# Kernel tuning notes

Measured on AMD Instinct MI355X. Metric: run time of the kernel, lower is better.

## Reference

```python
import jax, jax.numpy as jnp
import numpy as np

# fp4 e2m1 positive value grid and midpoints between adjacent grid values
_GRID = jnp.array([0.0, 0.5, 1.0, 1.5, 2.0, 3.0, 4.0, 6.0], dtype=jnp.float32)
_MIDS = jnp.array([0.25, 0.75, 1.25, 1.75, 2.5, 3.5, 5.0], dtype=jnp.float32)
BLOCK = 32               # MX block size
E8M0_BIAS = 127
F32_MIN_NORMAL = float(2.0 ** -126)
F4_E2M1_MAX_POW2 = 2     # log2 of largest power-of-two <= 6.0 -> 4.0


def _quantize_fp4(a):
    """Round-to-nearest-even onto the signed e2m1 grid."""
    mag = jnp.clip(jnp.abs(a), 0.0, 6.0)
    idx = jnp.searchsorted(_MIDS, mag, side='left')  # ties round down
    mids_pad = jnp.concatenate([_MIDS, jnp.array([-1.0], jnp.float32)])
    tie = mag == mids_pad[idx]
    idx = jnp.where(tie & (idx % 2 == 1), idx + 1, idx)  # ties-to-even mantissa
    return _GRID[idx] * jnp.where(a < 0, -1.0, 1.0)


def _floor_log2(m):
    """Exact floor(log2(m)) for m > 0, with corrections for fp rounding of log2."""
    e = jnp.floor(jnp.log2(m))
    e = jnp.where(jnp.exp2(e) > m, e - 1.0, e)
    e = jnp.where(jnp.exp2(e + 1.0) <= m, e + 1.0, e)
    return e


def _qdq_mxfp4(x):
    """Quantize-dequantize x to MX fp4_e2m1, block 32, FLOOR scale mode (to_mx + to_dtype)."""
    shp = x.shape
    xb = x.reshape(-1, BLOCK)
    max_abs = jnp.max(jnp.abs(xb), axis=1)
    eps = F32_MIN_NORMAL * (max_abs == 0).astype(jnp.float32)
    pow2 = _floor_log2(max_abs + eps)
    e_unb = jnp.clip(pow2 - F4_E2M1_MAX_POW2, -float(E8M0_BIAS), float(E8M0_BIAS) + 1.0)
    scale = jnp.maximum(jnp.exp2(e_unb), F32_MIN_NORMAL)  # [nblk]
    q = _quantize_fp4(xb / scale[:, None])
    return (q * scale[:, None]).reshape(shp)


def _dequant_weight(weight_packed, weight_scale, out_f, in_f):
    """Unpack uint8-packed fp4 (low nibble first), apply e8m0 block scales."""
    p = weight_packed.astype(jnp.int32)
    low = p & 0xF
    high = (p >> 4) & 0xF
    nib = jnp.stack([low, high], axis=-1).reshape(out_f, in_f)  # interleave low,high
    vals = _GRID[nib & 7] * jnp.where((nib & 8) > 0, -1.0, 1.0)
    s = jnp.exp2(weight_scale.astype(jnp.float32) - E8M0_BIAS)  # get_fp_scale(e8m0)
    return (vals.reshape(-1, BLOCK) * s[:, None]).reshape(out_f, in_f)


def setup_inputs() -> dict:
    key = jax.random.key(0)
    k1, k2, k3 = jax.random.split(key, 3)
    M, IN, OUT = 4096, 4096, 4096
    x = jax.random.normal(k1, (M, IN), dtype=jnp.float32)
    weight_packed = jax.random.randint(k2, (OUT, IN // 2), 0, 256, dtype=jnp.int32)
    weight_scale = jax.random.randint(k3, (OUT * IN // BLOCK,), 0, 135, dtype=jnp.int32)
    return {"x": x, "weight_packed": weight_packed, "weight_scale": weight_scale}


def reference(x, weight_packed, weight_scale):
    out_f = weight_packed.shape[0]
    in_f = weight_packed.shape[1] * 2
    xq = _qdq_mxfp4(x)                                       # qdq_mxfp4(x)
    w_dq = _dequant_weight(weight_packed, weight_scale, out_f, in_f)
    return xq @ w_dq.T                                       # matmul(x, w_dq.t())
```

## Files before the change

kernel.cpp:

```cpp
#include <hip/hip_runtime.h>
#include <stdint.h>

typedef __attribute__((ext_vector_type(4)))  int   intx4;
typedef __attribute__((ext_vector_type(8)))  int   intx8;
typedef __attribute__((ext_vector_type(16))) float floatx16;

#define GLL16(gp, lp)                                                               \
    __builtin_amdgcn_global_load_lds((const __attribute__((address_space(1))) unsigned int*)(gp), \
                                     (__attribute__((address_space(3))) unsigned int*)(lp), 16, 0, 0)
#define GLL4(gp, lp)                                                                \
    __builtin_amdgcn_global_load_lds((const __attribute__((address_space(1))) unsigned int*)(gp), \
                                     (__attribute__((address_space(3))) unsigned int*)(lp), 4, 0, 0)

__device__ __forceinline__ uint32_t enc1(float xv, float inv) {
    float a = fminf(fabsf(xv) * inv, 6.0f);
    int e;
    if (a < 2.0f)      e = (int)rintf(a + a);
    else if (a < 4.0f) e = (int)rintf(a) + 2;
    else               e = (int)rintf(a * 0.5f) + 4;
    return (uint32_t)e | ((__float_as_uint(xv) >> 28) & 8u);
}

__global__ __launch_bounds__(256) void quant_x_kernel(const float* __restrict__ x,
                                                      uint32_t* __restrict__ xq,
                                                      uint8_t* __restrict__ xs) {
    const int gl = blockIdx.x * 256 + threadIdx.x;
    const float4 v = ((const float4*)x)[gl];
    float m = fmaxf(fmaxf(fabsf(v.x), fabsf(v.y)), fmaxf(fabsf(v.z), fabsf(v.w)));
    m = fmaxf(m, __shfl_xor(m, 1));
    m = fmaxf(m, __shfl_xor(m, 2));
    m = fmaxf(m, __shfl_xor(m, 4));
    const unsigned ef = __float_as_uint(m) >> 23;
    const unsigned code = (ef < 3u) ? 1u : (ef - 2u);
    const float inv = __uint_as_float((254u - code) << 23);
    const uint32_t p = enc1(v.x, inv)        | (enc1(v.y, inv) << 4)
                     | (enc1(v.z, inv) << 8) | (enc1(v.w, inv) << 12);
    ((uint16_t*)xq)[gl] = (uint16_t)p;
    if ((gl & 7) == 0) xs[gl >> 3] = (uint8_t)code;
}

__global__ __launch_bounds__(256) void repack_kernel(const int* __restrict__ wp,
                                                     uint32_t* __restrict__ wrep,
                                                     int nwb,
                                                     const uint8_t* __restrict__ xs,
                                                     const int* __restrict__ wsc,
                                                     uint8_t* __restrict__ xs_t,
                                                     uint8_t* __restrict__ ws_t,
                                                     int R, int Ck) {
    const int bid = blockIdx.x;
    const int t = threadIdx.x;
    if (bid < nwb) {
        const int i = bid * 256 + t;
        const int4 p = ((const int4*)wp)[i];
        wrep[i] = (uint32_t)(p.x & 0xFF) | ((uint32_t)(p.y & 0xFF) << 8)
                | ((uint32_t)(p.z & 0xFF) << 16) | ((uint32_t)(p.w & 0xFF) << 24);
        return;
    }
    __shared__ uint8_t raw[128 * 32];
    const int tidx = bid - nwb;
    const int r0 = (tidx & 63) * 128;
    const int c0 = (tidx >> 6) * 32;
    const int r = t >> 1, hf = t & 1;
    if (r0 < R) {
        const uint4 v = *(const uint4*)(xs + (size_t)(r0 + r) * Ck + c0 + hf * 16);
        *(uint4*)(raw + r * 32 + hf * 16) = v;
    } else {
        const size_t base = (size_t)(r0 - R + r) * Ck + c0 + hf * 16;
        uint32_t b[4];
#pragma unroll
        for (int j = 0; j < 4; ++j) {
            const int4 p = *(const int4*)(wsc + base + 4 * j);
            b[j] = (uint32_t)(p.x & 0xFF) | ((uint32_t)(p.y & 0xFF) << 8)
                 | ((uint32_t)(p.z & 0xFF) << 16) | ((uint32_t)(p.w & 0xFF) << 24);
        }
        *(uint4*)(raw + r * 32 + hf * 16) = make_uint4(b[0], b[1], b[2], b[3]);
    }
    __syncthreads();
    const int c = t >> 3, q = t & 7;
    uint32_t d[4];
#pragma unroll
    for (int j = 0; j < 4; ++j) {
        const int mb = q * 16 + j * 4;
        d[j] = (uint32_t)raw[(mb + 0) * 32 + c]
             | ((uint32_t)raw[(mb + 1) * 32 + c] << 8)
             | ((uint32_t)raw[(mb + 2) * 32 + c] << 16)
             | ((uint32_t)raw[(mb + 3) * 32 + c] << 24);
    }
    uint8_t* outp = (r0 < R) ? (xs_t + (size_t)(c0 + c) * R + r0)
                             : (ws_t + (size_t)(c0 + c) * R + (r0 - R));
    *(uint4*)(outp + q * 16) = make_uint4(d[0], d[1], d[2], d[3]);
}

__global__ __launch_bounds__(256) void gemm_mx_kernel(const uint8_t* __restrict__ Apk,
                                                      const uint8_t* __restrict__ Bpk,
                                                      const uint8_t* __restrict__ AsT,
                                                      const uint8_t* __restrict__ BsT,
                                                      float* __restrict__ C,
                                                      int M, int N, int K) {
    __shared__ __align__(16) uint8_t sA[16384];
    __shared__ __align__(16) uint8_t sB[16384];
    __shared__ __align__(16) uint8_t sS[2048];

    const int tid = threadIdx.x;
    const int nwg = gridDim.x * gridDim.y;
    int bid = blockIdx.y * gridDim.x + blockIdx.x;
    bid = (bid & 7) * (nwg >> 3) + (bid >> 3);
    const int bn0 = (bid % gridDim.x) << 7;
    const int bm0 = (bid / gridDim.x) << 7;

    const int wave = tid >> 6;
    const int lane = tid & 63;
    const int wm = (wave >> 1) << 6;
    const int wn = (wave & 1) << 6;
    const int row = lane & 31;
    const int h = lane >> 5;
    const int Kb = K >> 1;

    const uint8_t* Ag[4];
    const uint8_t* Bg[4];
#pragma unroll
    for (int i = 0; i < 4; ++i) {
        const int s = tid + 256 * i;
        const int r = s >> 3;
        const int p = (s & 7) ^ (r & 7);
        Ag[i] = Apk + (size_t)(bm0 + r) * Kb + p * 16;
        Bg[i] = Bpk + (size_t)(bn0 + r) * Kb + p * 16;
    }

    const int st = tid & 127;
    const int sj = st >> 5, si = st & 31;
    const size_t sR = (size_t)((tid < 128) ? M : N);
    const uint8_t* Sg1 = ((tid < 128) ? (AsT + (size_t)sj * M + bm0)
                                      : (BsT + (size_t)sj * N + bn0)) + si * 4;
    const uint8_t* Sg2 = Sg1 + 4 * sR;
    const size_t sAdv = 8 * sR;
    const int soff = ((tid < 128) ? 0 : 1024) + st * 4;

    floatx16 acc[2][2];
#pragma unroll
    for (int a = 0; a < 2; ++a)
#pragma unroll
        for (int b = 0; b < 2; ++b)
#pragma unroll
            for (int r = 0; r < 16; ++r) acc[a][b][r] = 0.f;

    const int nchunk = K >> 8;
    const int ar0 = wm + row, ar1 = wm + 32 + row;
    const int br0 = wn + row, br1 = wn + 32 + row;

    for (int c = 0; c < nchunk; ++c) {
        __syncthreads();
        const size_t koff = (size_t)c << 7;
#pragma unroll
        for (int i = 0; i < 4; ++i) GLL16(Ag[i] + koff, sA + (tid + 256 * i) * 16);
#pragma unroll
        for (int i = 0; i < 4; ++i) GLL16(Bg[i] + koff, sB + (tid + 256 * i) * 16);
        GLL4(Sg1 + (size_t)c * sAdv, sS + soff);
        GLL4(Sg2 + (size_t)c * sAdv, sS + soff + 512);
        __syncthreads();

#pragma unroll
        for (int s = 0; s < 4; ++s) {
            const int kp = 2 * s + h;
            intx4 a4[2], b4[2];
            int sa[2], sb[2];
            a4[0] = *(const intx4*)(sA + ar0 * 128 + ((kp ^ (ar0 & 7)) << 4));
            a4[1] = *(const intx4*)(sA + ar1 * 128 + ((kp ^ (ar1 & 7)) << 4));
            b4[0] = *(const intx4*)(sB + br0 * 128 + ((kp ^ (br0 & 7)) << 4));
            b4[1] = *(const intx4*)(sB + br1 * 128 + ((kp ^ (br1 & 7)) << 4));
            sa[0] = sS[kp * 128 + ar0];
            sa[1] = sS[kp * 128 + ar1];
            sb[0] = sS[1024 + kp * 128 + br0];
            sb[1] = sS[1024 + kp * 128 + br1];
#pragma unroll
            for (int mt = 0; mt < 2; ++mt)
#pragma unroll
                for (int nt = 0; nt < 2; ++nt) {
                    intx8 a8 = {a4[mt][0], a4[mt][1], a4[mt][2], a4[mt][3], 0, 0, 0, 0};
                    intx8 b8 = {b4[nt][0], b4[nt][1], b4[nt][2], b4[nt][3], 0, 0, 0, 0};
                    acc[mt][nt] = __builtin_amdgcn_mfma_scale_f32_32x32x64_f8f6f4(
                        a8, b8, acc[mt][nt], 4, 4, 0, sa[mt], 0, sb[nt]);
                }
        }
    }

#pragma unroll
    for (int mt = 0; mt < 2; ++mt)
#pragma unroll
        for (int nt = 0; nt < 2; ++nt) {
            const int col = bn0 + wn + nt * 32 + row;
#pragma unroll
            for (int g = 0; g < 4; ++g) {
                const int rw = bm0 + wm + mt * 32 + 8 * g + 4 * h;
#pragma unroll
                for (int q = 0; q < 4; ++q)
                    C[(size_t)(rw + q) * N + col] = acc[mt][nt][4 * g + q];
            }
        }
}

extern "C" void kernel_launch(void* const* d_in, const int* in_sizes, int n_in,
                              void* d_out, int out_size, void* d_ws, size_t ws_size,
                              hipStream_t stream) {
    const float* x = (const float*)d_in[0];
    const int* wp = (const int*)d_in[1];
    const int* wsc = (const int*)d_in[2];
    float* out = (float*)d_out;

    const int K = 4096;
    const int M = in_sizes[0] / K;
    const int N = (in_sizes[1] * 2) / K;
    const int kbpr = K / 32;
    const int npack = N * K / 2;

    uint32_t* xq   = (uint32_t*)d_ws;
    uint8_t*  xs   = (uint8_t*)d_ws + (size_t)M * K / 2;
    uint32_t* wrep = (uint32_t*)(xs + (size_t)M * kbpr);
    uint8_t*  xs_t = (uint8_t*)(wrep + (size_t)npack / 4);
    uint8_t*  ws_t = xs_t + (size_t)M * kbpr;

    const int nwb = npack / 4 / 256;
    const int ntb = (2 * M / 128) * (kbpr / 32);

    quant_x_kernel<<<(M * K / 4) / 256, 256, 0, stream>>>(x, xq, xs);
    repack_kernel<<<nwb + ntb, 256, 0, stream>>>(wp, wrep, nwb,
                                                 xs, wsc, xs_t, ws_t, M, kbpr);

    dim3 grid(N / 128, M / 128);
    gemm_mx_kernel<<<grid, 256, 0, stream>>>((const uint8_t*)xq, (const uint8_t*)wrep,
                                             xs_t, ws_t, out, M, N, K);
}
```

Baseline: 199.6 us.

## Interleave scale layout so GEMM loads scales directly into registers

The x scales are now written in an interleaved per-row layout straight from the quantize kernel, so the x-scale transpose pass in the repack kernel goes away. The weight-scale repack produces the same layout. The GEMM reads each lane's scales with one 32-bit global load per 32-row tile per chunk, replacing the LDS staging buffer and byte LDS reads. The grouped block-index swizzle is also removed, which may change L2 reuse across workgroups.

Result: faster. 191.4 us (-4.1%).

```diff
diff --git a/kernel.cpp b/kernel.cpp
--- a/kernel.cpp
+++ b/kernel.cpp
@@ -8,9 +8,6 @@
 #define GLL16(gp, lp)                                                               \
     __builtin_amdgcn_global_load_lds((const __attribute__((address_space(1))) unsigned int*)(gp), \
                                      (__attribute__((address_space(3))) unsigned int*)(lp), 16, 0, 0)
-#define GLL4(gp, lp)                                                                \
-    __builtin_amdgcn_global_load_lds((const __attribute__((address_space(1))) unsigned int*)(gp), \
-                                     (__attribute__((address_space(3))) unsigned int*)(lp), 4, 0, 0)
 
 __device__ __forceinline__ uint32_t enc1(float xv, float inv) {
     float a = fminf(fabsf(xv) * inv, 6.0f);
@@ -23,7 +20,8 @@
 
 __global__ __launch_bounds__(256) void quant_x_kernel(const float* __restrict__ x,
                                                       uint32_t* __restrict__ xq,
-                                                      uint8_t* __restrict__ xs) {
+                                                      uint8_t* __restrict__ xsi,
+                                                      int M) {
     const int gl = blockIdx.x * 256 + threadIdx.x;
     const float4 v = ((const float4*)x)[gl];
     float m = fmaxf(fmaxf(fabsf(v.x), fabsf(v.y)), fmaxf(fabsf(v.z), fabsf(v.w)));
@@ -36,16 +34,19 @@
     const uint32_t p = enc1(v.x, inv)        | (enc1(v.y, inv) << 4)
                      | (enc1(v.z, inv) << 8) | (enc1(v.w, inv) << 12);
     ((uint16_t*)xq)[gl] = (uint16_t)p;
-    if ((gl & 7) == 0) xs[gl >> 3] = (uint8_t)code;
+    if ((gl & 7) == 0) {
+        const int blk = gl >> 3;
+        const int mm = blk >> 7, kb = blk & 127;
+        xsi[(size_t)(kb >> 3) * ((size_t)M * 8) + (size_t)mm * 8
+            + ((kb & 1) << 2) + ((kb & 7) >> 1)] = (uint8_t)code;
+    }
 }
 
 __global__ __launch_bounds__(256) void repack_kernel(const int* __restrict__ wp,
                                                      uint32_t* __restrict__ wrep,
                                                      int nwb,
-                                                     const uint8_t* __restrict__ xs,
                                                      const int* __restrict__ wsc,
-                                                     uint8_t* __restrict__ xs_t,
-                                                     uint8_t* __restrict__ ws_t,
+                                                     uint8_t* __restrict__ ws_i,
                                                      int R, int Ck) {
     const int bid = blockIdx.x;
     const int t = threadIdx.x;
@@ -58,14 +59,11 @@
     }
     __shared__ uint8_t raw[128 * 32];
     const int tidx = bid - nwb;
-    const int r0 = (tidx & 63) * 128;
-    const int c0 = (tidx >> 6) * 32;
-    const int r = t >> 1, hf = t & 1;
-    if (r0 < R) {
-        const uint4 v = *(const uint4*)(xs + (size_t)(r0 + r) * Ck + c0 + hf * 16);
-        *(uint4*)(raw + r * 32 + hf * 16) = v;
-    } else {
-        const size_t base = (size_t)(r0 - R + r) * Ck + c0 + hf * 16;
+    const int n0 = (tidx & 31) * 128;
+    const int c0 = (tidx >> 5) * 32;
+    {
+        const int r = t >> 1, hf = t & 1;
+        const size_t base = (size_t)(n0 + r) * Ck + c0 + hf * 16;
         uint32_t b[4];
 #pragma unroll
         for (int j = 0; j < 4; ++j) {
@@ -76,38 +74,32 @@
         *(uint4*)(raw + r * 32 + hf * 16) = make_uint4(b[0], b[1], b[2], b[3]);
     }
     __syncthreads();
-    const int c = t >> 3, q = t & 7;
-    uint32_t d[4];
-#pragma unroll
-    for (int j = 0; j < 4; ++j) {
-        const int mb = q * 16 + j * 4;
-        d[j] = (uint32_t)raw[(mb + 0) * 32 + c]
-             | ((uint32_t)raw[(mb + 1) * 32 + c] << 8)
-             | ((uint32_t)raw[(mb + 2) * 32 + c] << 16)
-             | ((uint32_t)raw[(mb + 3) * 32 + c] << 24);
-    }
-    uint8_t* outp = (r0 < R) ? (xs_t + (size_t)(c0 + c) * R + r0)
-                             : (ws_t + (size_t)(c0 + c) * R + (r0 - R));
-    *(uint4*)(outp + q * 16) = make_uint4(d[0], d[1], d[2], d[3]);
+    const int ml = t & 127;
+#pragma unroll
+    for (int pp = 0; pp < 2; ++pp) {
+        const int ckl = (t >> 7) + 2 * pp;
+        const int base = ml * 32 + ckl * 8;
+        const uint32_t lo = (uint32_t)raw[base + 0] | ((uint32_t)raw[base + 2] << 8)
+                          | ((uint32_t)raw[base + 4] << 16) | ((uint32_t)raw[base + 6] << 24);
+        const uint32_t hi = (uint32_t)raw[base + 1] | ((uint32_t)raw[base + 3] << 8)
+                          | ((uint32_t)raw[base + 5] << 16) | ((uint32_t)raw[base + 7] << 24);
+        *(uint2*)(ws_i + (size_t)(c0 / 8 + ckl) * ((size_t)R * 8)
+                       + (size_t)(n0 + ml) * 8) = make_uint2(lo, hi);
+    }
 }
 
 __global__ __launch_bounds__(256) void gemm_mx_kernel(const uint8_t* __restrict__ Apk,
                                                       const uint8_t* __restrict__ Bpk,
-                                                      const uint8_t* __restrict__ AsT,
-                                                      const uint8_t* __restrict__ BsT,
+                                                      const uint8_t* __restrict__ Asi,
+                                                      const uint8_t* __restrict__ Bsi,
                                                       float* __restrict__ C,
                                                       int M, int N, int K) {
     __shared__ __align__(16) uint8_t sA[16384];
     __shared__ __align__(16) uint8_t sB[16384];
-    __shared__ __align__(16) uint8_t sS[2048];
 
     const int tid = threadIdx.x;
-    const int nwg = gridDim.x * gridDim.y;
-    int bid = blockIdx.y * gridDim.x + blockIdx.x;
-    bid = (bid & 7) * (nwg >> 3) + (bid >> 3);
-    const int bn0 = (bid % gridDim.x) << 7;
-    const int bm0 = (bid / gridDim.x) << 7;
-
+    const int bm0 = blockIdx.y << 7;
+    const int bn0 = blockIdx.x << 7;
     const int wave = tid >> 6;
     const int lane = tid & 63;
     const int wm = (wave >> 1) << 6;
@@ -127,26 +119,25 @@
         Bg[i] = Bpk + (size_t)(bn0 + r) * Kb + p * 16;
     }
 
-    const int st = tid & 127;
-    const int sj = st >> 5, si = st & 31;
-    const size_t sR = (size_t)((tid < 128) ? M : N);
-    const uint8_t* Sg1 = ((tid < 128) ? (AsT + (size_t)sj * M + bm0)
-                                      : (BsT + (size_t)sj * N + bn0)) + si * 4;
-    const uint8_t* Sg2 = Sg1 + 4 * sR;
-    const size_t sAdv = 8 * sR;
-    const int soff = ((tid < 128) ? 0 : 1024) + st * 4;
-
-    floatx16 acc[2][2];
-#pragma unroll
-    for (int a = 0; a < 2; ++a)
-#pragma unroll
-        for (int b = 0; b < 2; ++b)
-#pragma unroll
-            for (int r = 0; r < 16; ++r) acc[a][b][r] = 0.f;
-
-    const int nchunk = K >> 8;
     const int ar0 = wm + row, ar1 = wm + 32 + row;
     const int br0 = wn + row, br1 = wn + 32 + row;
+
+    const uint8_t* SgA0 = Asi + (size_t)(bm0 + ar0) * 8 + h * 4;
+    const uint8_t* SgA1 = Asi + (size_t)(bm0 + ar1) * 8 + h * 4;
+    const uint8_t* SgB0 = Bsi + (size_t)(bn0 + br0) * 8 + h * 4;
+    const uint8_t* SgB1 = Bsi + (size_t)(bn0 + br1) * 8 + h * 4;
+    const size_t sStepA = (size_t)M * 8;
+    const size_t sStepB = (size_t)N * 8;
+
+    floatx16 acc[2][2];
+#pragma unroll
+    for (int a = 0; a < 2; ++a)
+#pragma unroll
+        for (int b = 0; b < 2; ++b)
+#pragma unroll
+            for (int r = 0; r < 16; ++r) acc[a][b][r] = 0.f;
+
+    const int nchunk = K >> 8;
 
     for (int c = 0; c < nchunk; ++c) {
         __syncthreads();
@@ -155,23 +146,25 @@
         for (int i = 0; i < 4; ++i) GLL16(Ag[i] + koff, sA + (tid + 256 * i) * 16);
 #pragma unroll
         for (int i = 0; i < 4; ++i) GLL16(Bg[i] + koff, sB + (tid + 256 * i) * 16);
-        GLL4(Sg1 + (size_t)c * sAdv, sS + soff);
-        GLL4(Sg2 + (size_t)c * sAdv, sS + soff + 512);
+        uint32_t sa32[2], sb32[2];
+        sa32[0] = *(const uint32_t*)(SgA0 + c * sStepA);
+        sa32[1] = *(const uint32_t*)(SgA1 + c * sStepA);
+        sb32[0] = *(const uint32_t*)(SgB0 + c * sStepB);
+        sb32[1] = *(const uint32_t*)(SgB1 + c * sStepB);
         __syncthreads();
 
 #pragma unroll
         for (int s = 0; s < 4; ++s) {
             const int kp = 2 * s + h;
             intx4 a4[2], b4[2];
-            int sa[2], sb[2];
             a4[0] = *(const intx4*)(sA + ar0 * 128 + ((kp ^ (ar0 & 7)) << 4));
             a4[1] = *(const intx4*)(sA + ar1 * 128 + ((kp ^ (ar1 & 7)) << 4));
             b4[0] = *(const intx4*)(sB + br0 * 128 + ((kp ^ (br0 & 7)) << 4));
             b4[1] = *(const intx4*)(sB + br1 * 128 + ((kp ^ (br1 & 7)) << 4));
-            sa[0] = sS[kp * 128 + ar0];
-            sa[1] = sS[kp * 128 + ar1];
-            sb[0] = sS[1024 + kp * 128 + br0];
-            sb[1] = sS[1024 + kp * 128 + br1];
+            const int sa[2] = { (int)((sa32[0] >> (8 * s)) & 0xFF),
+                                (int)((sa32[1] >> (8 * s)) & 0xFF) };
+            const int sb[2] = { (int)((sb32[0] >> (8 * s)) & 0xFF),
+                                (int)((sb32[1] >> (8 * s)) & 0xFF) };
 #pragma unroll
             for (int mt = 0; mt < 2; ++mt)
 #pragma unroll
@@ -214,19 +207,17 @@
     const int npack = N * K / 2;
 
     uint32_t* xq   = (uint32_t*)d_ws;
-    uint8_t*  xs   = (uint8_t*)d_ws + (size_t)M * K / 2;
-    uint32_t* wrep = (uint32_t*)(xs + (size_t)M * kbpr);
-    uint8_t*  xs_t = (uint8_t*)(wrep + (size_t)npack / 4);
-    uint8_t*  ws_t = xs_t + (size_t)M * kbpr;
+    uint8_t*  xs_i = (uint8_t*)d_ws + (size_t)M * K / 2;
+    uint32_t* wrep = (uint32_t*)(xs_i + (size_t)M * kbpr);
+    uint8_t*  ws_i = (uint8_t*)(wrep + (size_t)npack / 4);
 
     const int nwb = npack / 4 / 256;
-    const int ntb = (2 * M / 128) * (kbpr / 32);
-
-    quant_x_kernel<<<(M * K / 4) / 256, 256, 0, stream>>>(x, xq, xs);
-    repack_kernel<<<nwb + ntb, 256, 0, stream>>>(wp, wrep, nwb,
-                                                 xs, wsc, xs_t, ws_t, M, kbpr);
+    const int ntb = (N / 128) * (kbpr / 32);
+
+    quant_x_kernel<<<(M * K / 4) / 256, 256, 0, stream>>>(x, xq, xs_i, M);
+    repack_kernel<<<nwb + ntb, 256, 0, stream>>>(wp, wrep, nwb, wsc, ws_i, N, kbpr);
 
     dim3 grid(N / 128, M / 128);
     gemm_mx_kernel<<<grid, 256, 0, stream>>>((const uint8_t*)xq, (const uint8_t*)wrep,
-                                             xs_t, ws_t, out, M, N, K);
-}
+                                             xs_i, ws_i, out, M, N, K);
+}
```

## Fuse x quantization and weight repack into one prep kernel, drop tile swizzle

Applied to the files above, without the earlier changes.

Merges the x-quantization kernel and the repack kernel into a single launch. The x scales are now written directly in transposed layout, which removes the separate transpose pass over x scales and one kernel boundary. The GEMM's block-index remapping (grouped-by-8 swizzle) is also removed in favor of plain row-major tile order. The transposed scale store is a scattered byte write with stride M, and dropping the swizzle may hurt L2 reuse in the GEMM.

After: 183.0 us. -8.4%, faster.

```diff
diff --git a/kernel.cpp b/kernel.cpp
--- a/kernel.cpp
+++ b/kernel.cpp
@@ -21,51 +21,51 @@
     return (uint32_t)e | ((__float_as_uint(xv) >> 28) & 8u);
 }
 
-__global__ __launch_bounds__(256) void quant_x_kernel(const float* __restrict__ x,
-                                                      uint32_t* __restrict__ xq,
-                                                      uint8_t* __restrict__ xs) {
-    const int gl = blockIdx.x * 256 + threadIdx.x;
-    const float4 v = ((const float4*)x)[gl];
-    float m = fmaxf(fmaxf(fabsf(v.x), fabsf(v.y)), fmaxf(fabsf(v.z), fabsf(v.w)));
-    m = fmaxf(m, __shfl_xor(m, 1));
-    m = fmaxf(m, __shfl_xor(m, 2));
-    m = fmaxf(m, __shfl_xor(m, 4));
-    const unsigned ef = __float_as_uint(m) >> 23;
-    const unsigned code = (ef < 3u) ? 1u : (ef - 2u);
-    const float inv = __uint_as_float((254u - code) << 23);
-    const uint32_t p = enc1(v.x, inv)        | (enc1(v.y, inv) << 4)
-                     | (enc1(v.z, inv) << 8) | (enc1(v.w, inv) << 12);
-    ((uint16_t*)xq)[gl] = (uint16_t)p;
-    if ((gl & 7) == 0) xs[gl >> 3] = (uint8_t)code;
-}
-
-__global__ __launch_bounds__(256) void repack_kernel(const int* __restrict__ wp,
-                                                     uint32_t* __restrict__ wrep,
-                                                     int nwb,
-                                                     const uint8_t* __restrict__ xs,
-                                                     const int* __restrict__ wsc,
-                                                     uint8_t* __restrict__ xs_t,
-                                                     uint8_t* __restrict__ ws_t,
-                                                     int R, int Ck) {
+__global__ __launch_bounds__(256) void prep_kernel(const float* __restrict__ x,
+                                                   uint32_t* __restrict__ xq,
+                                                   uint8_t* __restrict__ xs_t,
+                                                   int nq, int M,
+                                                   const int* __restrict__ wp,
+                                                   uint32_t* __restrict__ wrep,
+                                                   int nwb,
+                                                   const int* __restrict__ wsc,
+                                                   uint8_t* __restrict__ ws_t,
+                                                   int N, int Ck) {
     const int bid = blockIdx.x;
     const int t = threadIdx.x;
-    if (bid < nwb) {
-        const int i = bid * 256 + t;
+    if (bid < nq) {
+        const int gl = bid * 256 + t;
+        const float4 v = ((const float4*)x)[gl];
+        float m = fmaxf(fmaxf(fabsf(v.x), fabsf(v.y)), fmaxf(fabsf(v.z), fabsf(v.w)));
+        m = fmaxf(m, __shfl_xor(m, 1));
+        m = fmaxf(m, __shfl_xor(m, 2));
+        m = fmaxf(m, __shfl_xor(m, 4));
+        const unsigned ef = __float_as_uint(m) >> 23;
+        const unsigned code = (ef < 3u) ? 1u : (ef - 2u);
+        const float inv = __uint_as_float((254u - code) << 23);
+        const uint32_t p = enc1(v.x, inv)        | (enc1(v.y, inv) << 4)
+                         | (enc1(v.z, inv) << 8) | (enc1(v.w, inv) << 12);
+        ((uint16_t*)xq)[gl] = (uint16_t)p;
+        if ((gl & 7) == 0) {
+            const int blk = gl >> 3;
+            xs_t[(size_t)(blk & 127) * M + (blk >> 7)] = (uint8_t)code;
+        }
+        return;
+    }
+    if (bid < nq + nwb) {
+        const int i = (bid - nq) * 256 + t;
         const int4 p = ((const int4*)wp)[i];
         wrep[i] = (uint32_t)(p.x & 0xFF) | ((uint32_t)(p.y & 0xFF) << 8)
                 | ((uint32_t)(p.z & 0xFF) << 16) | ((uint32_t)(p.w & 0xFF) << 24);
         return;
     }
     __shared__ uint8_t raw[128 * 32];
-    const int tidx = bid - nwb;
-    const int r0 = (tidx & 63) * 128;
-    const int c0 = (tidx >> 6) * 32;
-    const int r = t >> 1, hf = t & 1;
-    if (r0 < R) {
-        const uint4 v = *(const uint4*)(xs + (size_t)(r0 + r) * Ck + c0 + hf * 16);
-        *(uint4*)(raw + r * 32 + hf * 16) = v;
-    } else {
-        const size_t base = (size_t)(r0 - R + r) * Ck + c0 + hf * 16;
+    const int tidx = bid - nq - nwb;
+    const int n0 = (tidx & 31) * 128;
+    const int c0 = (tidx >> 5) * 32;
+    {
+        const int r = t >> 1, hf = t & 1;
+        const size_t base = (size_t)(n0 + r) * Ck + c0 + hf * 16;
         uint32_t b[4];
 #pragma unroll
         for (int j = 0; j < 4; ++j) {
@@ -86,9 +86,7 @@
              | ((uint32_t)raw[(mb + 2) * 32 + c] << 16)
              | ((uint32_t)raw[(mb + 3) * 32 + c] << 24);
     }
-    uint8_t* outp = (r0 < R) ? (xs_t + (size_t)(c0 + c) * R + r0)
-                             : (ws_t + (size_t)(c0 + c) * R + (r0 - R));
-    *(uint4*)(outp + q * 16) = make_uint4(d[0], d[1], d[2], d[3]);
+    *(uint4*)(ws_t + (size_t)(c0 + c) * N + n0 + q * 16) = make_uint4(d[0], d[1], d[2], d[3]);
 }
 
 __global__ __launch_bounds__(256) void gemm_mx_kernel(const uint8_t* __restrict__ Apk,
@@ -102,12 +100,8 @@
     __shared__ __align__(16) uint8_t sS[2048];
 
     const int tid = threadIdx.x;
-    const int nwg = gridDim.x * gridDim.y;
-    int bid = blockIdx.y * gridDim.x + blockIdx.x;
-    bid = (bid & 7) * (nwg >> 3) + (bid >> 3);
-    const int bn0 = (bid % gridDim.x) << 7;
-    const int bm0 = (bid / gridDim.x) << 7;
-
+    const int bm0 = blockIdx.y << 7;
+    const int bn0 = blockIdx.x << 7;
     const int wave = tid >> 6;
     const int lane = tid & 63;
     const int wm = (wave >> 1) << 6;
@@ -214,17 +208,17 @@
     const int npack = N * K / 2;
 
     uint32_t* xq   = (uint32_t*)d_ws;
-    uint8_t*  xs   = (uint8_t*)d_ws + (size_t)M * K / 2;
-    uint32_t* wrep = (uint32_t*)(xs + (size_t)M * kbpr);
-    uint8_t*  xs_t = (uint8_t*)(wrep + (size_t)npack / 4);
-    uint8_t*  ws_t = xs_t + (size_t)M * kbpr;
-
+    uint8_t*  xs_t = (uint8_t*)d_ws + (size_t)M * K / 2;
+    uint32_t* wrep = (uint32_t*)(xs_t + (size_t)M * kbpr);
+    uint8_t*  ws_t = (uint8_t*)(wrep + (size_t)npack / 4);
+
+    const int nq  = (M * K / 4) / 256;
     const int nwb = npack / 4 / 256;
-    const int ntb = (2 * M / 128) * (kbpr / 32);
-
-    quant_x_kernel<<<(M * K / 4) / 256, 256, 0, stream>>>(x, xq, xs);
-    repack_kernel<<<nwb + ntb, 256, 0, stream>>>(wp, wrep, nwb,
-                                                 xs, wsc, xs_t, ws_t, M, kbpr);
+    const int ntb = (N / 128) * (kbpr / 32);
+
+    prep_kernel<<<nq + nwb + ntb, 256, 0, stream>>>(x, xq, xs_t, nq, M,
+                                                    wp, wrep, nwb,
+                                                    wsc, ws_t, N, kbpr);
 
     dim3 grid(N / 128, M / 128);
     gemm_mx_kernel<<<grid, 256, 0, stream>>>((const uint8_t*)xq, (const uint8_t*)wrep,
```
